# Kernel optimization log

Measured on AMD Instinct MI355X. Metric: run time of the kernel, lower is better.

The kernel has to match this reference:

```python
import jax, jax.numpy as jnp
import numpy as np

DIM = 768
HEADS = 12
DIM_HEAD = 64
INNER = HEADS * DIM_HEAD  # 768
SCALE = DIM_HEAD ** -0.5


def setup_inputs() -> dict:
    key = jax.random.key(0)
    k1, k2, k3, k4 = jax.random.split(key, 4)
    b, n = 8, 1024
    x = jax.random.normal(k1, (b, n, DIM), dtype=jnp.float32)
    # fused QKV projection, no bias: y = x @ w_qkv  -> [b, n, 3*inner]
    w_qkv = jax.random.normal(k2, (DIM, 3 * INNER), dtype=jnp.float32) * (DIM ** -0.5)
    # output projection with bias
    w_out = jax.random.normal(k3, (INNER, DIM), dtype=jnp.float32) * (INNER ** -0.5)
    b_out = jax.random.normal(k4, (DIM,), dtype=jnp.float32) * 0.02
    return {"x": x, "w_qkv": w_qkv, "w_out": w_out, "b_out": b_out}


def reference(x, w_qkv, w_out, b_out):
    b, n, _ = x.shape
    qkv = jnp.einsum('bnd,de->bne', x, w_qkv)  # [b, n, 3*inner]
    q, k, v = jnp.split(qkv, 3, axis=-1)
    # 'b n (h d) -> b h n d'
    def split_heads(t):
        return t.reshape(b, n, HEADS, DIM_HEAD).transpose(0, 2, 1, 3)
    q, k, v = split_heads(q), split_heads(k), split_heads(v)
    dots = jnp.einsum('bhid,bhjd->bhij', q, k) * SCALE  # [b, h, n, n]
    attn = jax.nn.softmax(dots, axis=-1)
    out = jnp.einsum('bhij,bhjd->bhid', attn, v)  # [b, h, n, d]
    out = out.transpose(0, 2, 1, 3).reshape(b, n, INNER)  # 'b h n d -> b n (h d)'
    return jnp.einsum('bne,ed->bnd', out, w_out) + b_out
```

## Files before the change

### kernel.cpp

```cpp
#include <hip/hip_runtime.h>

typedef unsigned short u16;
typedef __bf16 bf16x8 __attribute__((ext_vector_type(8)));
typedef float f32x4 __attribute__((ext_vector_type(4)));

__device__ inline u16 f2bf(float f) {
    union { float f; unsigned int u; } a; a.f = f;
    unsigned int u = a.u + 0x7fffu + ((a.u >> 16) & 1u);
    return (u16)(u >> 16);
}
__device__ __forceinline__ float truncbf(float f, u16& h) {
    union { float f; unsigned int u; } a; a.f = f;
    a.u &= 0xffff0000u;
    h = (u16)(a.u >> 16);
    return a.f;
}

__device__ __forceinline__ void cp16(const void* g, void* l) {
    __builtin_amdgcn_global_load_lds(
        (const __attribute__((address_space(1))) unsigned int*)g,
        (__attribute__((address_space(3))) unsigned int*)l, 16, 0, 0);
}

__global__ __launch_bounds__(256) void prep(
    const float* __restrict__ x, const float* __restrict__ wq,
    const float* __restrict__ wo, u16* __restrict__ xbf,
    u16* __restrict__ wtq, u16* __restrict__ wto)
{
    int bid = blockIdx.x;
    if (bid < 3072) {
        size_t base = ((size_t)bid * 256 + threadIdx.x) * 8;
        float4 f0 = *(const float4*)&x[base];
        float4 f1 = *(const float4*)&x[base + 4];
        union { u16 s[8]; uint4 v; } t;
        t.s[0]=f2bf(f0.x); t.s[1]=f2bf(f0.y); t.s[2]=f2bf(f0.z); t.s[3]=f2bf(f0.w);
        t.s[4]=f2bf(f1.x); t.s[5]=f2bf(f1.y); t.s[6]=f2bf(f1.z); t.s[7]=f2bf(f1.w);
        *(uint4*)&xbf[base] = t.v;
        return;
    }
    __shared__ u16 tile[32][33];
    const float* in; u16* outp; int N, bx, by;
    if (bid < 3072 + 1728) { int t = bid - 3072; in = wq; outp = wtq; N = 2304; bx = t % 72; by = t / 72; }
    else                   { int t = bid - 4800; in = wo; outp = wto; N = 768;  bx = t % 24; by = t / 24; }
    int n0 = bx * 32, k0 = by * 32;
    int tx = threadIdx.x & 31, ty = threadIdx.x >> 5;
    #pragma unroll
    for (int r = ty; r < 32; r += 8)
        tile[r][tx] = f2bf(in[(size_t)(k0 + r) * N + n0 + tx]);
    __syncthreads();
    #pragma unroll
    for (int r = ty; r < 32; r += 8)
        outp[(size_t)(n0 + r) * 768 + k0 + tx] = tile[tx][r];
}

__global__ __launch_bounds__(256) void gemm_qkv(
    const u16* __restrict__ A, const u16* __restrict__ Bt,
    u16* __restrict__ q_out, u16* __restrict__ k_out, u16* __restrict__ v_out)
{
    const int K = 768;
    __shared__ __align__(16) u16 As[2][128 * 64];
    __shared__ __align__(16) u16 Bs[2][128 * 64];

    int tid = threadIdx.x;
    int lane = tid & 63, wave = tid >> 6;
    int quad = lane >> 4, l16 = lane & 15;
    int wm = wave >> 1, wn = wave & 1;
    int id = blockIdx.x;
    int xcd = id & 7, j = id >> 3;
    int m0 = (((j & 7) << 3) + xcd) * 128;
    int n0 = (j >> 3) * 128;

    f32x4 acc[4][4];
    #pragma unroll
    for (int i = 0; i < 4; i++)
        #pragma unroll
        for (int jj = 0; jj < 4; jj++) acc[i][jj] = (f32x4){0.f, 0.f, 0.f, 0.f};

    int r0 = tid >> 3, cg = tid & 7;
    int g = cg ^ (r0 & 7);
    const u16* GA[4]; const u16* GB[4];
    #pragma unroll
    for (int it = 0; it < 4; it++) {
        GA[it] = A  + (size_t)(m0 + it * 32 + r0) * K + g * 8;
        GB[it] = Bt + (size_t)(n0 + it * 32 + r0) * K + g * 8;
    }

    #define STAGE_QKV(kt, b)                                          \
        _Pragma("unroll")                                             \
        for (int it = 0; it < 4; it++) {                              \
            cp16(GA[it] + (kt), &As[b][(it * 256 + tid) * 8]);        \
            cp16(GB[it] + (kt), &Bs[b][(it * 256 + tid) * 8]);        \
        }

    STAGE_QKV(0, 0)
    for (int i = 0; i < 12; i++) {
        int b = i & 1;
        __syncthreads();
        bf16x8 af[2][4], bfr[2][4];
        #pragma unroll
        for (int ko = 0; ko < 2; ko++)
            #pragma unroll
            for (int x = 0; x < 4; x++) {
                int Ra = wm * 64 + x * 16 + l16;
                af[ko][x]  = *(const bf16x8*)&As[b][Ra * 64 + (((ko * 4 + quad) ^ (Ra & 7)) * 8)];
                int Rb = wn * 64 + x * 16 + l16;
                bfr[ko][x] = *(const bf16x8*)&Bs[b][Rb * 64 + (((ko * 4 + quad) ^ (Rb & 7)) * 8)];
            }
        if (i + 1 < 12) { STAGE_QKV((i + 1) * 64, b ^ 1) }
        #pragma unroll
        for (int ko = 0; ko < 2; ko++)
            #pragma unroll
            for (int x = 0; x < 4; x++)
                #pragma unroll
                for (int y = 0; y < 4; y++)
                    acc[x][y] = __builtin_amdgcn_mfma_f32_16x16x32_bf16(af[ko][x], bfr[ko][y], acc[x][y], 0, 0, 0);
    }
    #undef STAGE_QKV

    int M0 = m0 + wm * 64, N0 = n0 + wn * 64;
    int part = N0 >= 1536 ? 2 : (N0 >= 768 ? 1 : 0);
    int h = (N0 - part * 768) >> 6;
    int b2 = M0 >> 10, npos0 = M0 & 1023;
    u16* ep = (wave < 2 ? As[0] : Bs[0]) + (wave & 1) * 4096;

    if (part != 2) {
        float scale = (part == 0) ? 0.18033688011112042f : 1.0f;
        u16* gbase = (part == 0 ? q_out : k_out) + (((size_t)(b2 * 12 + h) * 1024 + npos0) << 6);
        #pragma unroll
        for (int i = 0; i < 4; i++)
            #pragma unroll
            for (int jj = 0; jj < 4; jj++) {
                int dd = jj * 16 + l16;
                #pragma unroll
                for (int r = 0; r < 4; r++) {
                    int np = i * 16 + quad * 4 + r;
                    ep[np * 64 + (((dd >> 3) ^ (np & 7)) * 8) + (dd & 7)] =
                        f2bf(acc[i][jj][r] * scale);
                }
            }
        #pragma unroll
        for (int t = 0; t < 8; t++) {
            int idx = t * 512 + lane * 8;
            int np = idx >> 6;
            int slot = ((lane & 7) ^ (np & 7));
            uint4 v = *(const uint4*)&ep[np * 64 + slot * 8];
            *(uint4*)&gbase[idx] = v;
        }
    } else {
        #pragma unroll
        for (int i = 0; i < 4; i++)
            #pragma unroll
            for (int jj = 0; jj < 4; jj++) {
                int dd = jj * 16 + l16;
                int npg = i * 2 + (quad >> 1);
                int sub = (quad & 1) * 4;
                union { u16 s[4]; uint2 v; } pk;
                #pragma unroll
                for (int r = 0; r < 4; r++) pk.s[r] = f2bf(acc[i][jj][r]);
                *(uint2*)&ep[dd * 64 + ((npg ^ (dd & 7)) * 8) + sub] = pk.v;
            }
        #pragma unroll
        for (int t = 0; t < 8; t++) {
            int dd = t * 8 + (lane >> 3);
            int npg = lane & 7;
            uint4 v = *(const uint4*)&ep[dd * 64 + ((npg ^ (dd & 7)) * 8)];
            *(uint4*)&v_out[((size_t)((b2 * 12 + h) * 64 + dd)) * 1024 + npos0 + npg * 8] = v;
        }
    }
}

__global__ __launch_bounds__(256) void attn128(
    u16* __restrict__ QO, const u16* __restrict__ Kg, const u16* __restrict__ Vtg)
{
    __shared__ __align__(16) u16 Ks[2][64 * 64];
    __shared__ __align__(16) u16 Vs[2][64 * 64];

    int tid = threadIdx.x;
    int lane = tid & 63, wave = tid >> 6;
    int quad = lane >> 4, l16 = lane & 15;
    int id = blockIdx.x;
    int xcd = id & 7, j = id >> 3;
    int bh = xcd * 12 + (j >> 3);
    int q0 = (j & 7) * 128;
    const size_t head_base = (size_t)bh * 65536;

    size_t qoff[2];
    bf16x8 qf[2][2];
    #pragma unroll
    for (int qs = 0; qs < 2; qs++) {
        qoff[qs] = head_base + (size_t)(q0 + wave * 32 + qs * 16 + l16) * 64;
        qf[qs][0] = *(const bf16x8*)&QO[qoff[qs] + quad * 8];
        qf[qs][1] = *(const bf16x8*)&QO[qoff[qs] + 32 + quad * 8];
    }

    f32x4 Oacc[4][2];
    #pragma unroll
    for (int dt = 0; dt < 4; dt++)
        #pragma unroll
        for (int qs = 0; qs < 2; qs++) Oacc[dt][qs] = (f32x4){0.f, 0.f, 0.f, 0.f};
    float l_part[2] = {0.f, 0.f};

    int srow = tid >> 3, sg = tid & 7;
    int gs = sg ^ (srow & 7);
    const u16* GK[2]; const u16* GV[2];
    #pragma unroll
    for (int it = 0; it < 2; it++) {
        GK[it] = Kg  + head_base + (size_t)(it * 32 + srow) * 64 + gs * 8;
        GV[it] = Vtg + head_base + (size_t)(it * 32 + srow) * 1024 + gs * 8;
    }

    #define STAGE_ATT(j0, b)                                          \
        _Pragma("unroll")                                             \
        for (int it = 0; it < 2; it++) {                              \
            cp16(GK[it] + (size_t)(j0) * 64, &Ks[b][(it * 256 + tid) * 8]); \
            cp16(GV[it] + (j0),             &Vs[b][(it * 256 + tid) * 8]); \
        }

    STAGE_ATT(0, 0)
    for (int i = 0; i < 16; i++) {
        int b = i & 1;
        __syncthreads();
        bf16x8 kf[4][2];
        #pragma unroll
        for (int nt = 0; nt < 4; nt++) {
            int R = nt * 16 + l16;
            kf[nt][0] = *(const bf16x8*)&Ks[b][R * 64 + ((quad       ^ (R & 7)) * 8)];
            kf[nt][1] = *(const bf16x8*)&Ks[b][R * 64 + (((quad + 4) ^ (R & 7)) * 8)];
        }
        if (i + 1 < 16) { STAGE_ATT((i + 1) * 64, b ^ 1) }

        f32x4 s4[4][2];
        #pragma unroll
        for (int nt = 0; nt < 4; nt++)
            #pragma unroll
            for (int qs = 0; qs < 2; qs++) {
                f32x4 s = (f32x4){0.f, 0.f, 0.f, 0.f};
                s = __builtin_amdgcn_mfma_f32_16x16x32_bf16(kf[nt][0], qf[qs][0], s, 0, 0, 0);
                s = __builtin_amdgcn_mfma_f32_16x16x32_bf16(kf[nt][1], qf[qs][1], s, 0, 0, 0);
                s4[nt][qs] = s;
            }

        u16 ph[4][2][4];
        #pragma unroll
        for (int nt = 0; nt < 4; nt++)
            #pragma unroll
            for (int qs = 0; qs < 2; qs++)
                #pragma unroll
                for (int r = 0; r < 4; r++) {
                    float p = __builtin_amdgcn_exp2f(s4[nt][qs][r]);
                    l_part[qs] += truncbf(p, ph[nt][qs][r]);
                }

        #pragma unroll
        for (int h = 0; h < 2; h++) {
            union { u16 s[8]; bf16x8 v; } pk[2];
            #pragma unroll
            for (int qs = 0; qs < 2; qs++)
                #pragma unroll
                for (int r = 0; r < 4; r++) {
                    pk[qs].s[r]     = ph[2 * h][qs][r];
                    pk[qs].s[4 + r] = ph[2 * h + 1][qs][r];
                }
            int lg0 = 4 * h + (quad >> 1), lg1 = lg0 + 2;
            int off = (quad & 1) * 4;
            #pragma unroll
            for (int dt = 0; dt < 4; dt++) {
                int drow = dt * 16 + l16;
                union { u16 s[8]; bf16x8 v; } vk;
                *(uint2*)&vk.s[0] = *(const uint2*)&Vs[b][drow * 64 + (lg0 ^ (drow & 7)) * 8 + off];
                *(uint2*)&vk.s[4] = *(const uint2*)&Vs[b][drow * 64 + (lg1 ^ (drow & 7)) * 8 + off];
                #pragma unroll
                for (int qs = 0; qs < 2; qs++)
                    Oacc[dt][qs] = __builtin_amdgcn_mfma_f32_16x16x32_bf16(vk.v, pk[qs].v, Oacc[dt][qs], 0, 0, 0);
            }
        }
    }
    #undef STAGE_ATT

    #pragma unroll
    for (int qs = 0; qs < 2; qs++) {
        float l = l_part[qs];
        l += __shfl_xor(l, 16);
        l += __shfl_xor(l, 32);
        float rl = __builtin_amdgcn_rcpf(l);
        #pragma unroll
        for (int dt = 0; dt < 4; dt++) {
            union { u16 s[4]; uint2 v; } ok;
            #pragma unroll
            for (int r = 0; r < 4; r++) ok.s[r] = f2bf(Oacc[dt][qs][r] * rl);
            *(uint2*)&QO[qoff[qs] + dt * 16 + quad * 4] = ok.v;
        }
    }
}

__global__ __launch_bounds__(256) void gemm_out(
    const u16* __restrict__ Qg, const u16* __restrict__ Bt,
    const float* __restrict__ bias, float* __restrict__ out)
{
    const int K = 768;
    __shared__ __align__(16) u16 As[2][128 * 64];
    __shared__ __align__(16) u16 Bs[2][128 * 64];

    int tid = threadIdx.x;
    int lane = tid & 63, wave = tid >> 6;
    int quad = lane >> 4, l16 = lane & 15;
    int wm = wave >> 1, wn = wave & 1;
    int id = blockIdx.x;
    int xcd = id & 7, j = id >> 3;
    int m0 = (((j & 7) << 3) + xcd) * 128;
    int n0 = (j >> 3) * 128;

    f32x4 acc[4][4];
    #pragma unroll
    for (int i = 0; i < 4; i++)
        #pragma unroll
        for (int jj = 0; jj < 4; jj++) acc[i][jj] = (f32x4){0.f, 0.f, 0.f, 0.f};

    int r0 = tid >> 3, cg = tid & 7;
    int g = cg ^ (r0 & 7);
    const u16* GA[4]; const u16* GB[4];
    #pragma unroll
    for (int it = 0; it < 4; it++) {
        int m = m0 + it * 32 + r0, b = m >> 10, npos = m & 1023;
        GA[it] = Qg + (((size_t)(b * 12) * 1024 + npos) << 6) + g * 8;
        GB[it] = Bt + (size_t)(n0 + it * 32 + r0) * K + g * 8;
    }

    #define STAGE_OUT(i2, b)                                              \
        _Pragma("unroll")                                                 \
        for (int it = 0; it < 4; it++) {                                  \
            cp16(GA[it] + (size_t)(i2) * 65536, &As[b][(it * 256 + tid) * 8]); \
            cp16(GB[it] + (i2) * 64,            &Bs[b][(it * 256 + tid) * 8]); \
        }

    STAGE_OUT(0, 0)
    for (int i = 0; i < 12; i++) {
        int b = i & 1;
        __syncthreads();
        bf16x8 af[2][4], bfr[2][4];
        #pragma unroll
        for (int ko = 0; ko < 2; ko++)
            #pragma unroll
            for (int x = 0; x < 4; x++) {
                int Ra = wm * 64 + x * 16 + l16;
                af[ko][x]  = *(const bf16x8*)&As[b][Ra * 64 + (((ko * 4 + quad) ^ (Ra & 7)) * 8)];
                int Rb = wn * 64 + x * 16 + l16;
                bfr[ko][x] = *(const bf16x8*)&Bs[b][Rb * 64 + (((ko * 4 + quad) ^ (Rb & 7)) * 8)];
            }
        if (i + 1 < 12) { STAGE_OUT(i + 1, b ^ 1) }
        #pragma unroll
        for (int ko = 0; ko < 2; ko++)
            #pragma unroll
            for (int x = 0; x < 4; x++)
                #pragma unroll
                for (int y = 0; y < 4; y++)
                    acc[x][y] = __builtin_amdgcn_mfma_f32_16x16x32_bf16(af[ko][x], bfr[ko][y], acc[x][y], 0, 0, 0);
    }
    #undef STAGE_OUT

    #pragma unroll
    for (int i = 0; i < 4; i++) {
        int mbase = m0 + wm * 64 + i * 16 + quad * 4;
        #pragma unroll
        for (int jj = 0; jj < 4; jj++) {
            int n = n0 + wn * 64 + jj * 16 + l16;
            float bv = bias[n];
            #pragma unroll
            for (int r = 0; r < 4; r++)
                out[(size_t)(mbase + r) * 768 + n] = acc[i][jj][r] + bv;
        }
    }
}

extern "C" void kernel_launch(void* const* d_in, const int* in_sizes, int n_in,
                              void* d_out, int out_size, void* d_ws, size_t ws_size,
                              hipStream_t stream) {
    const float* x     = (const float*)d_in[0];
    const float* w_qkv = (const float*)d_in[1];
    const float* w_out = (const float*)d_in[2];
    const float* b_out = (const float*)d_in[3];
    float* out = (float*)d_out;

    char* ws = (char*)d_ws;
    u16* wtq  = (u16*)(ws);
    u16* wto  = (u16*)(ws + 3538944);
    u16* Qbuf = (u16*)(ws + 4718592);
    u16* xbf  = (u16*)(ws + 17301504);
    u16* Kbuf = (u16*)d_out;
    u16* Vbuf = (u16*)d_out + 6291456;

    prep<<<dim3(5376), 256, 0, stream>>>(x, w_qkv, w_out, xbf, wtq, wto);
    gemm_qkv<<<dim3(1152), 256, 0, stream>>>(xbf, wtq, Qbuf, Kbuf, Vbuf);
    attn128<<<dim3(768), 256, 0, stream>>>(Qbuf, Kbuf, Vbuf);
    gemm_out<<<dim3(384), 256, 0, stream>>>(Qbuf, wto, b_out, out);
}
```

Baseline: 183.7 us.

## Halve QKV GEMM K-tile to shrink LDS and issue async loads earlier

The QKV projection GEMM now stages 32-wide K slices instead of 64, with a new packed swizzled LDS layout that places two 64-row halves side by side. This halves its shared memory (from 64KB to 32KB) so more blocks can be resident per CU, at the cost of twice as many loop iterations and barriers. The epilogue staging pointer is remapped to fit the smaller buffers, and a barrier is added before the epilogue. In the QKV, attention and output GEMM loops, the next-tile async global-to-LDS copy is now issued right after the barrier, before the current tile's LDS fragment reads, giving the loads more time to overlap compute.

```diff
diff --git a/kernel.cpp b/kernel.cpp
--- a/kernel.cpp
+++ b/kernel.cpp
@@ -58,8 +58,8 @@
     u16* __restrict__ q_out, u16* __restrict__ k_out, u16* __restrict__ v_out)
 {
     const int K = 768;
-    __shared__ __align__(16) u16 As[2][128 * 64];
-    __shared__ __align__(16) u16 Bs[2][128 * 64];
+    __shared__ __align__(16) u16 As[2][128 * 32];
+    __shared__ __align__(16) u16 Bs[2][128 * 32];
 
     int tid = threadIdx.x;
     int lane = tid & 63, wave = tid >> 6;
@@ -76,52 +76,53 @@
         #pragma unroll
         for (int jj = 0; jj < 4; jj++) acc[i][jj] = (f32x4){0.f, 0.f, 0.f, 0.f};
 
-    int r0 = tid >> 3, cg = tid & 7;
-    int g = cg ^ (r0 & 7);
-    const u16* GA[4]; const u16* GB[4];
-    #pragma unroll
-    for (int it = 0; it < 4; it++) {
-        GA[it] = A  + (size_t)(m0 + it * 32 + r0) * K + g * 8;
-        GB[it] = Bt + (size_t)(n0 + it * 32 + r0) * K + g * 8;
-    }
-
-    #define STAGE_QKV(kt, b)                                          \
-        _Pragma("unroll")                                             \
-        for (int it = 0; it < 4; it++) {                              \
-            cp16(GA[it] + (kt), &As[b][(it * 256 + tid) * 8]);        \
-            cp16(GB[it] + (kt), &Bs[b][(it * 256 + tid) * 8]);        \
-        }
-
-    STAGE_QKV(0, 0)
-    for (int i = 0; i < 12; i++) {
+    const u16* GA[2]; const u16* GB[2];
+    #pragma unroll
+    for (int it = 0; it < 2; it++) {
+        int c = it * 256 + tid;
+        int rp = c >> 3;
+        int t8 = (c & 7) ^ (rp & 7);
+        int row = rp + 64 * (t8 >> 2), gk = t8 & 3;
+        GA[it] = A  + (size_t)(m0 + row) * K + gk * 8;
+        GB[it] = Bt + (size_t)(n0 + row) * K + gk * 8;
+    }
+
+    #define STG(kt, b)                                              \
+        _Pragma("unroll")                                           \
+        for (int it = 0; it < 2; it++) {                            \
+            cp16(GA[it] + (kt), &As[b][(it * 256 + tid) * 8]);      \
+            cp16(GB[it] + (kt), &Bs[b][(it * 256 + tid) * 8]);      \
+        }
+
+    STG(0, 0)
+    for (int i = 0; i < 24; i++) {
         int b = i & 1;
         __syncthreads();
-        bf16x8 af[2][4], bfr[2][4];
-        #pragma unroll
-        for (int ko = 0; ko < 2; ko++)
-            #pragma unroll
-            for (int x = 0; x < 4; x++) {
-                int Ra = wm * 64 + x * 16 + l16;
-                af[ko][x]  = *(const bf16x8*)&As[b][Ra * 64 + (((ko * 4 + quad) ^ (Ra & 7)) * 8)];
-                int Rb = wn * 64 + x * 16 + l16;
-                bfr[ko][x] = *(const bf16x8*)&Bs[b][Rb * 64 + (((ko * 4 + quad) ^ (Rb & 7)) * 8)];
-            }
-        if (i + 1 < 12) { STAGE_QKV((i + 1) * 64, b ^ 1) }
-        #pragma unroll
-        for (int ko = 0; ko < 2; ko++)
-            #pragma unroll
-            for (int x = 0; x < 4; x++)
-                #pragma unroll
-                for (int y = 0; y < 4; y++)
-                    acc[x][y] = __builtin_amdgcn_mfma_f32_16x16x32_bf16(af[ko][x], bfr[ko][y], acc[x][y], 0, 0, 0);
-    }
-    #undef STAGE_QKV
+        if (i + 1 < 24) { STG((i + 1) * 32, b ^ 1) }
+        bf16x8 af[4], bfr[4];
+        #pragma unroll
+        for (int x = 0; x < 4; x++) {
+            int Ra = wm * 64 + x * 16 + l16, ra = Ra & 63;
+            int sa = (((Ra >> 6) << 2) + quad) ^ (ra & 7);
+            af[x] = *(const bf16x8*)&As[b][ra * 64 + sa * 8];
+            int Rb = wn * 64 + x * 16 + l16, rb = Rb & 63;
+            int sb = (((Rb >> 6) << 2) + quad) ^ (rb & 7);
+            bfr[x] = *(const bf16x8*)&Bs[b][rb * 64 + sb * 8];
+        }
+        #pragma unroll
+        for (int x = 0; x < 4; x++)
+            #pragma unroll
+            for (int y = 0; y < 4; y++)
+                acc[x][y] = __builtin_amdgcn_mfma_f32_16x16x32_bf16(af[x], bfr[y], acc[x][y], 0, 0, 0);
+    }
+    #undef STG
+    __syncthreads();
 
     int M0 = m0 + wm * 64, N0 = n0 + wn * 64;
     int part = N0 >= 1536 ? 2 : (N0 >= 768 ? 1 : 0);
     int h = (N0 - part * 768) >> 6;
     int b2 = M0 >> 10, npos0 = M0 & 1023;
-    u16* ep = (wave < 2 ? As[0] : Bs[0]) + (wave & 1) * 4096;
+    u16* ep = (wave & 2) ? &Bs[wave & 1][0] : &As[wave & 1][0];
 
     if (part != 2) {
         float scale = (part == 0) ? 0.18033688011112042f : 1.0f;
@@ -220,6 +221,7 @@
     for (int i = 0; i < 16; i++) {
         int b = i & 1;
         __syncthreads();
+        if (i + 1 < 16) { STAGE_ATT((i + 1) * 64, b ^ 1) }
         bf16x8 kf[4][2];
         #pragma unroll
         for (int nt = 0; nt < 4; nt++) {
@@ -227,7 +229,6 @@
             kf[nt][0] = *(const bf16x8*)&Ks[b][R * 64 + ((quad       ^ (R & 7)) * 8)];
             kf[nt][1] = *(const bf16x8*)&Ks[b][R * 64 + (((quad + 4) ^ (R & 7)) * 8)];
         }
-        if (i + 1 < 16) { STAGE_ATT((i + 1) * 64, b ^ 1) }
 
         f32x4 s4[4][2];
         #pragma unroll
@@ -337,6 +338,7 @@
     for (int i = 0; i < 12; i++) {
         int b = i & 1;
         __syncthreads();
+        if (i + 1 < 12) { STAGE_OUT(i + 1, b ^ 1) }
         bf16x8 af[2][4], bfr[2][4];
         #pragma unroll
         for (int ko = 0; ko < 2; ko++)
@@ -347,7 +349,6 @@
                 int Rb = wn * 64 + x * 16 + l16;
                 bfr[ko][x] = *(const bf16x8*)&Bs[b][Rb * 64 + (((ko * 4 + quad) ^ (Rb & 7)) * 8)];
             }
-        if (i + 1 < 12) { STAGE_OUT(i + 1, b ^ 1) }
         #pragma unroll
         for (int ko = 0; ko < 2; ko++)
             #pragma unroll
```

New measurement: 193.0 us. 5.1% more time.
